# Kernel tuning notes

Hardware: AMD Instinct MI355X
Metric: run time of the kernel (lower is better)

Reference implementation:

```python
import jax, jax.numpy as jnp
import numpy as np

T = 8192
F = 128   # feature_size
H = 2048  # hidden_size
PRED_LEN = 12  # pred_length (fc_out head exists in module but is unused in forward)


def setup_inputs() -> dict:
    key = jax.random.key(0)
    ks = jax.random.split(key, 10)
    s_ih = 1.0 / np.sqrt(H)
    inp = {
        "x": jax.random.normal(ks[0], (T, F), dtype=jnp.float32),
        # PyTorch nn.LSTM params, gate order [i, f, g, o]
        "W_ih": jax.random.uniform(ks[1], (4 * H, F), jnp.float32, -s_ih, s_ih),
        "W_hh": jax.random.uniform(ks[2], (4 * H, H), jnp.float32, -s_ih, s_ih),
        "b_ih": jax.random.uniform(ks[3], (4 * H,), jnp.float32, -s_ih, s_ih),
        "b_hh": jax.random.uniform(ks[4], (4 * H,), jnp.float32, -s_ih, s_ih),
        # self.linear: Linear(H, H)
        "W_lin": jax.random.uniform(ks[5], (H, H), jnp.float32, -s_ih, s_ih),
        "b_lin": jax.random.uniform(ks[6], (H,), jnp.float32, -s_ih, s_ih),
        # self.one_out: Linear(H, 2)
        "W_out": jax.random.uniform(ks[7], (2, H), jnp.float32, -s_ih, s_ih),
        "b_out": jax.random.uniform(ks[8], (2,), jnp.float32, -s_ih, s_ih),
    }
    return inp


def _lstm_last_h(x, W_ih, W_hh, b_ih, b_hh):
    # x: [T, F]; returns final hidden state h: [H]
    # Precompute input projections for all timesteps: [T, 4H]
    x_proj = x @ W_ih.T + (b_ih + b_hh)

    def step(carry, xp):
        h, c = carry
        gates = xp + h @ W_hh.T  # [4H]
        i = jax.nn.sigmoid(gates[0 * H:1 * H])
        f = jax.nn.sigmoid(gates[1 * H:2 * H])
        g = jnp.tanh(gates[2 * H:3 * H])
        o = jax.nn.sigmoid(gates[3 * H:4 * H])
        c = f * c + i * g
        h = o * jnp.tanh(c)
        return (h, c), None

    h0 = jnp.zeros((H,), x.dtype)
    c0 = jnp.zeros((H,), x.dtype)
    (h, _), _ = jax.lax.scan(step, (h0, c0), x_proj)
    return h


def reference(x, W_ih, W_hh, b_ih, b_hh, W_lin, b_lin, W_out, b_out):
    h = _lstm_last_h(x, W_ih, W_hh, b_ih, b_hh)        # [H]
    y = h @ W_lin.T + b_lin                            # [H]
    y = y @ W_out.T + b_out                            # [2]
    return y.reshape(1, 1, 2)                          # matches torch (1,1,2)
```

## Files before the change

kernel.cpp:

```cpp
#include <hip/hip_runtime.h>


#define H      2048
#define TSTEPS 8192
#define FEAT   128
#define NBLK   256
#define NTHR   512

typedef float vf4 __attribute__((ext_vector_type(4)));
typedef float vf2 __attribute__((ext_vector_type(2)));
typedef unsigned long long u64;
typedef unsigned int u32;

__device__ __forceinline__ float sigm(float xv) {
  return __builtin_amdgcn_rcpf(1.0f + __expf(-xv));
}
__device__ __forceinline__ float tanh_(float xv) {
  return 1.0f - 2.0f * __builtin_amdgcn_rcpf(__expf(2.0f * xv) + 1.0f);
}

__device__ __forceinline__ u64 aload64(const u64* p) {
  return __hip_atomic_load(p, __ATOMIC_RELAXED, __HIP_MEMORY_SCOPE_AGENT);
}
__device__ __forceinline__ u32 aload32(const u32* p) {
  return __hip_atomic_load(p, __ATOMIC_RELAXED, __HIP_MEMORY_SCOPE_AGENT);
}
__device__ __forceinline__ void astoref(float* p, float v) {
  __hip_atomic_store(p, v, __ATOMIC_RELAXED, __HIP_MEMORY_SCOPE_AGENT);
}
__device__ __forceinline__ void astoreu(u32* p, u32 v) {
  __hip_atomic_store(p, v, __ATOMIC_RELAXED, __HIP_MEMORY_SCOPE_AGENT);
}

#define DECLG(g) vf4 w##g##_0, w##g##_1, w##g##_2, w##g##_3, \
                     w##g##_4, w##g##_5, w##g##_6, w##g##_7; \
                 vf2 wih##g; float bias##g; float acc##g;

#define LOADG(g) { \
  const int row_ = (g) * H + j; \
  const float* wr_ = W_hh + (long)row_ * H; \
  w##g##_0 = *(const vf4*)(wr_ + 4*(ln      )); \
  w##g##_1 = *(const vf4*)(wr_ + 4*(ln +  64)); \
  w##g##_2 = *(const vf4*)(wr_ + 4*(ln + 128)); \
  w##g##_3 = *(const vf4*)(wr_ + 4*(ln + 192)); \
  w##g##_4 = *(const vf4*)(wr_ + 4*(ln + 256)); \
  w##g##_5 = *(const vf4*)(wr_ + 4*(ln + 320)); \
  w##g##_6 = *(const vf4*)(wr_ + 4*(ln + 384)); \
  w##g##_7 = *(const vf4*)(wr_ + 4*(ln + 448)); \
  wih##g  = *(const vf2*)(W_ih + (long)row_ * FEAT + 2*ln); \
  bias##g = b_ih[row_] + b_hh[row_]; }

#define PIN(g) asm volatile("" : \
  "+v"(w##g##_0), "+v"(w##g##_1), "+v"(w##g##_2), "+v"(w##g##_3), \
  "+v"(w##g##_4), "+v"(w##g##_5), "+v"(w##g##_6), "+v"(w##g##_7), \
  "+v"(wih##g), "+v"(bias##g));

#define LDSREAD(k, ldsrow) \
  const vf4 hv##k = *(const vf4*)&(ldsrow)[4*(ln + 64*(k))];

#define FMA_G(g, c) \
  acc##g = __builtin_fmaf(w##g##_##c.x, h4_.x, acc##g); \
  acc##g = __builtin_fmaf(w##g##_##c.y, h4_.y, acc##g); \
  acc##g = __builtin_fmaf(w##g##_##c.z, h4_.z, acc##g); \
  acc##g = __builtin_fmaf(w##g##_##c.w, h4_.w, acc##g);

#define FMA_C(c) { const vf4 h4_ = hv##c; \
  FMA_G(0, c) FMA_G(1, c) FMA_G(2, c) FMA_G(3, c) }

#define REDUCE(g) { float a_ = acc##g; \
  a_ += __shfl_xor(a_, 1);  a_ += __shfl_xor(a_, 2);  a_ += __shfl_xor(a_, 4); \
  a_ += __shfl_xor(a_, 8);  a_ += __shfl_xor(a_, 16); a_ += __shfl_xor(a_, 32); \
  acc##g = a_ + bias##g; }

__device__ __forceinline__ void poll_and_stage(const u32* __restrict__ slots,
                                               const float* __restrict__ hsrc,
                                               int tgt,
                                               float* __restrict__ ldsrow,
                                               int wv, int ln) {
  const u32* sp = slots + wv * 32 + (ln & 31);
  int v = (int)aload32(sp);
  while (!__all((ln < 32) ? (v >= tgt) : 1)) {
    __builtin_amdgcn_s_sleep(1);
    if ((ln < 32) && (v < tgt)) v = (int)aload32(sp);
  }
  const int base = wv * 256 + 4 * ln;
  const u64* hp = (const u64*)(hsrc + base);
  const u64 d0 = aload64(hp);
  const u64 d1 = aload64(hp + 1);
  vf4 hv;
  hv.x = __uint_as_float((u32)d0);
  hv.y = __uint_as_float((u32)(d0 >> 32));
  hv.z = __uint_as_float((u32)d1);
  hv.w = __uint_as_float((u32)(d1 >> 32));
  *(vf4*)&ldsrow[base] = hv;
}

__global__ __launch_bounds__(NTHR, 2)
void lstm_persist(const float* __restrict__ x,
                  const float* __restrict__ W_ih,
                  const float* __restrict__ W_hh,
                  const float* __restrict__ b_ih,
                  const float* __restrict__ b_hh,
                  const float* __restrict__ W_lin,
                  const float* __restrict__ b_lin,
                  const float* __restrict__ W_out,
                  const float* __restrict__ b_out,
                  float* __restrict__ out,
                  float* __restrict__ ws)
{
  const int tid = threadIdx.x;
  const int b   = blockIdx.x;
  const int wv  = tid >> 6;
  const int ln  = tid & 63;

  float* hbuf0 = ws;
  float* hbuf1 = ws + H;
  u32*   slots = (u32*)(ws + 2 * H);

  __shared__ __align__(16) float h_lds[2][H];

  *(vf4*)&h_lds[0][4 * tid] = (vf4)(0.0f);

  const int j = b * 8 + wv;
  DECLG(0) DECLG(1) DECLG(2) DECLG(3)
  LOADG(0) LOADG(1) LOADG(2) LOADG(3)
  PIN(0) PIN(1) PIN(2) PIN(3)

  __syncthreads();

  float cst = 0.0f;

  #pragma unroll 1
  for (int t = 0; t < TSTEPS; ++t) {
    const vf2 xr = *(const vf2*)(x + (long)t * FEAT + 2 * ln);
    float* ldsrow = h_lds[t & 1];

    if (t > 0)
      poll_and_stage(slots, (t & 1) ? hbuf1 : hbuf0, t, ldsrow, wv, ln);
    __syncthreads();

    LDSREAD(0, ldsrow) LDSREAD(1, ldsrow) LDSREAD(2, ldsrow) LDSREAD(3, ldsrow)
    LDSREAD(4, ldsrow) LDSREAD(5, ldsrow) LDSREAD(6, ldsrow) LDSREAD(7, ldsrow)

    acc0 = wih0.x * xr.x + wih0.y * xr.y;
    acc1 = wih1.x * xr.x + wih1.y * xr.y;
    acc2 = wih2.x * xr.x + wih2.y * xr.y;
    acc3 = wih3.x * xr.x + wih3.y * xr.y;

    FMA_C(0) FMA_C(1) FMA_C(2) FMA_C(3)
    FMA_C(4) FMA_C(5) FMA_C(6) FMA_C(7)

    REDUCE(0) REDUCE(1) REDUCE(2) REDUCE(3)

    const float iv = sigm(acc0);
    const float fv = sigm(acc1);
    const float gv = tanh_(acc2);
    const float ov = sigm(acc3);
    cst = fv * cst + iv * gv;
    const float hval = ov * tanh_(cst);

    if (ln == 0)
      astoref((((t + 1) & 1) ? hbuf1 : hbuf0) + j, hval);

    __syncthreads();
    if (tid == 0)
      astoreu(slots + b, (u32)(t + 1));
  }

  {
    float* ldsrow = h_lds[0];
    poll_and_stage(slots, hbuf0, TSTEPS, ldsrow, wv, ln);
    __syncthreads();

    float a0 = 0.0f;
    const float* wl = W_lin + (long)j * H;
    #pragma unroll
    for (int k = 0; k < 8; ++k) {
      const vf4 h4 = *(const vf4*)&ldsrow[4 * (ln + 64 * k)];
      const vf4 u  = *(const vf4*)(wl + 4 * (ln + 64 * k));
      a0 += u.x * h4.x + u.y * h4.y + u.z * h4.z + u.w * h4.w;
    }
    a0 += __shfl_xor(a0, 1);  a0 += __shfl_xor(a0, 2);  a0 += __shfl_xor(a0, 4);
    a0 += __shfl_xor(a0, 8);  a0 += __shfl_xor(a0, 16); a0 += __shfl_xor(a0, 32);

    if (ln == 0)
      astoref(hbuf1 + j, a0 + b_lin[j]);
    __syncthreads();
    if (tid == 0)
      astoreu(slots + b, (u32)(TSTEPS + 1));
  }

  if (b == 0 && wv == 0) {
    const u32* sp = slots + 4 * ln;
    int v0 = (int)aload32(sp + 0), v1 = (int)aload32(sp + 1);
    int v2 = (int)aload32(sp + 2), v3 = (int)aload32(sp + 3);
    const int tgt = TSTEPS + 1;
    while (!__all((v0 >= tgt) & (v1 >= tgt) & (v2 >= tgt) & (v3 >= tgt))) {
      __builtin_amdgcn_s_sleep(1);
      if (v0 < tgt) v0 = (int)aload32(sp + 0);
      if (v1 < tgt) v1 = (int)aload32(sp + 1);
      if (v2 < tgt) v2 = (int)aload32(sp + 2);
      if (v3 < tgt) v3 = (int)aload32(sp + 3);
    }
    float p0 = 0.0f, p1 = 0.0f;
    #pragma unroll
    for (int k = 0; k < 16; ++k) {
      const u64 d  = aload64((const u64*)hbuf1 + ln + 64 * k);
      const int c  = 2 * (ln + 64 * k);
      const float ylo = __uint_as_float((u32)d);
      const float yhi = __uint_as_float((u32)(d >> 32));
      p0 = __builtin_fmaf(W_out[c],         ylo, p0);
      p0 = __builtin_fmaf(W_out[c + 1],     yhi, p0);
      p1 = __builtin_fmaf(W_out[H + c],     ylo, p1);
      p1 = __builtin_fmaf(W_out[H + c + 1], yhi, p1);
    }
    p0 += __shfl_xor(p0, 1);  p0 += __shfl_xor(p0, 2);  p0 += __shfl_xor(p0, 4);
    p0 += __shfl_xor(p0, 8);  p0 += __shfl_xor(p0, 16); p0 += __shfl_xor(p0, 32);
    p1 += __shfl_xor(p1, 1);  p1 += __shfl_xor(p1, 2);  p1 += __shfl_xor(p1, 4);
    p1 += __shfl_xor(p1, 8);  p1 += __shfl_xor(p1, 16); p1 += __shfl_xor(p1, 32);
    if (ln == 0) {
      out[0] = p0 + b_out[0];
      out[1] = p1 + b_out[1];
    }
  }
}

extern "C" void kernel_launch(void* const* d_in, const int* in_sizes, int n_in,
                              void* d_out, int out_size, void* d_ws, size_t ws_size,
                              hipStream_t stream) {
  const float* x     = (const float*)d_in[0];
  const float* W_ih  = (const float*)d_in[1];
  const float* W_hh  = (const float*)d_in[2];
  const float* b_ih  = (const float*)d_in[3];
  const float* b_hh  = (const float*)d_in[4];
  const float* W_lin = (const float*)d_in[5];
  const float* b_lin = (const float*)d_in[6];
  const float* W_out = (const float*)d_in[7];
  const float* b_out = (const float*)d_in[8];

  lstm_persist<<<dim3(NBLK), dim3(NTHR), 0, stream>>>(
      x, W_ih, W_hh, b_ih, b_hh, W_lin, b_lin, W_out, b_out,
      (float*)d_out, (float*)d_ws);
}
```

Baseline: 34.44 ms.

## Replace per-block flags with step-tagged 64-bit hidden-state entries

Each hidden value is now written together with its timestep tag as one 64-bit atomic store. Consumers poll the tagged data directly instead of first polling per-block flags and then reading the data. This drops the per-step block barrier and the separate flag store, cutting one dependent global round trip from the critical path of every recurrent step. In exchange, each wave's polling now reads 4 u64 per lane instead of one u32, which raises spin traffic to L2, and the workspace footprint doubles.

Result: slower. 48.50 ms (+40.8%).

```diff
diff --git a/kernel.cpp b/kernel.cpp
--- a/kernel.cpp
+++ b/kernel.cpp
@@ -22,14 +22,13 @@
 __device__ __forceinline__ u64 aload64(const u64* p) {
   return __hip_atomic_load(p, __ATOMIC_RELAXED, __HIP_MEMORY_SCOPE_AGENT);
 }
-__device__ __forceinline__ u32 aload32(const u32* p) {
-  return __hip_atomic_load(p, __ATOMIC_RELAXED, __HIP_MEMORY_SCOPE_AGENT);
-}
-__device__ __forceinline__ void astoref(float* p, float v) {
+__device__ __forceinline__ void astore64(u64* p, u64 v) {
   __hip_atomic_store(p, v, __ATOMIC_RELAXED, __HIP_MEMORY_SCOPE_AGENT);
 }
-__device__ __forceinline__ void astoreu(u32* p, u32 v) {
-  __hip_atomic_store(p, v, __ATOMIC_RELAXED, __HIP_MEMORY_SCOPE_AGENT);
+__device__ __forceinline__ int  tag_of(u64 d) { return (int)(u32)(d >> 32); }
+__device__ __forceinline__ float val_of(u64 d) { return __uint_as_float((u32)d); }
+__device__ __forceinline__ u64  pack(int tag, float v) {
+  return ((u64)(u32)tag << 32) | (u64)__float_as_uint(v);
 }
 
 #define DECLG(g) vf4 w##g##_0, w##g##_1, w##g##_2, w##g##_3, \
@@ -72,27 +71,29 @@
   a_ += __shfl_xor(a_, 8);  a_ += __shfl_xor(a_, 16); a_ += __shfl_xor(a_, 32); \
   acc##g = a_ + bias##g; }
 
-__device__ __forceinline__ void poll_and_stage(const u32* __restrict__ slots,
-                                               const float* __restrict__ hsrc,
-                                               int tgt,
-                                               float* __restrict__ ldsrow,
-                                               int wv, int ln) {
-  const u32* sp = slots + wv * 32 + (ln & 31);
-  int v = (int)aload32(sp);
-  while (!__all((ln < 32) ? (v >= tgt) : 1)) {
+__device__ __forceinline__ void poll_stage(const u64* __restrict__ pq,
+                                           int tgt,
+                                           float* __restrict__ ldsrow,
+                                           int wv, int ln) {
+  const u64* hp = pq + wv * 256 + 4 * ln;
+  u64 d0 = aload64(hp + 0);
+  u64 d1 = aload64(hp + 1);
+  u64 d2 = aload64(hp + 2);
+  u64 d3 = aload64(hp + 3);
+  while (!__all((tag_of(d0) >= tgt) & (tag_of(d1) >= tgt) &
+                (tag_of(d2) >= tgt) & (tag_of(d3) >= tgt))) {
     __builtin_amdgcn_s_sleep(1);
-    if ((ln < 32) && (v < tgt)) v = (int)aload32(sp);
-  }
-  const int base = wv * 256 + 4 * ln;
-  const u64* hp = (const u64*)(hsrc + base);
-  const u64 d0 = aload64(hp);
-  const u64 d1 = aload64(hp + 1);
+    if (tag_of(d0) < tgt) d0 = aload64(hp + 0);
+    if (tag_of(d1) < tgt) d1 = aload64(hp + 1);
+    if (tag_of(d2) < tgt) d2 = aload64(hp + 2);
+    if (tag_of(d3) < tgt) d3 = aload64(hp + 3);
+  }
   vf4 hv;
-  hv.x = __uint_as_float((u32)d0);
-  hv.y = __uint_as_float((u32)(d0 >> 32));
-  hv.z = __uint_as_float((u32)d1);
-  hv.w = __uint_as_float((u32)(d1 >> 32));
-  *(vf4*)&ldsrow[base] = hv;
+  hv.x = val_of(d0);
+  hv.y = val_of(d1);
+  hv.z = val_of(d2);
+  hv.w = val_of(d3);
+  *(vf4*)&ldsrow[wv * 256 + 4 * ln] = hv;
 }
 
 __global__ __launch_bounds__(NTHR, 2)
@@ -113,9 +114,7 @@
   const int wv  = tid >> 6;
   const int ln  = tid & 63;
 
-  float* hbuf0 = ws;
-  float* hbuf1 = ws + H;
-  u32*   slots = (u32*)(ws + 2 * H);
+  u64* hq = (u64*)ws;
 
   __shared__ __align__(16) float h_lds[2][H];
 
@@ -136,7 +135,7 @@
     float* ldsrow = h_lds[t & 1];
 
     if (t > 0)
-      poll_and_stage(slots, (t & 1) ? hbuf1 : hbuf0, t, ldsrow, wv, ln);
+      poll_stage(hq + (t & 1) * H, t, ldsrow, wv, ln);
     __syncthreads();
 
     LDSREAD(0, ldsrow) LDSREAD(1, ldsrow) LDSREAD(2, ldsrow) LDSREAD(3, ldsrow)
@@ -160,16 +159,12 @@
     const float hval = ov * tanh_(cst);
 
     if (ln == 0)
-      astoref((((t + 1) & 1) ? hbuf1 : hbuf0) + j, hval);
-
-    __syncthreads();
-    if (tid == 0)
-      astoreu(slots + b, (u32)(t + 1));
+      astore64(hq + ((t + 1) & 1) * H + j, pack(t + 1, hval));
   }
 
   {
     float* ldsrow = h_lds[0];
-    poll_and_stage(slots, hbuf0, TSTEPS, ldsrow, wv, ln);
+    poll_stage(hq, TSTEPS, ldsrow, wv, ln);
     __syncthreads();
 
     float a0 = 0.0f;
@@ -184,35 +179,39 @@
     a0 += __shfl_xor(a0, 8);  a0 += __shfl_xor(a0, 16); a0 += __shfl_xor(a0, 32);
 
     if (ln == 0)
-      astoref(hbuf1 + j, a0 + b_lin[j]);
-    __syncthreads();
-    if (tid == 0)
-      astoreu(slots + b, (u32)(TSTEPS + 1));
+      astore64(hq + H + j, pack(TSTEPS + 1, a0 + b_lin[j]));
   }
 
   if (b == 0 && wv == 0) {
-    const u32* sp = slots + 4 * ln;
-    int v0 = (int)aload32(sp + 0), v1 = (int)aload32(sp + 1);
-    int v2 = (int)aload32(sp + 2), v3 = (int)aload32(sp + 3);
+    const u64* yq = hq + H;
     const int tgt = TSTEPS + 1;
-    while (!__all((v0 >= tgt) & (v1 >= tgt) & (v2 >= tgt) & (v3 >= tgt))) {
-      __builtin_amdgcn_s_sleep(1);
-      if (v0 < tgt) v0 = (int)aload32(sp + 0);
-      if (v1 < tgt) v1 = (int)aload32(sp + 1);
-      if (v2 < tgt) v2 = (int)aload32(sp + 2);
-      if (v3 < tgt) v3 = (int)aload32(sp + 3);
-    }
     float p0 = 0.0f, p1 = 0.0f;
-    #pragma unroll
-    for (int k = 0; k < 16; ++k) {
-      const u64 d  = aload64((const u64*)hbuf1 + ln + 64 * k);
-      const int c  = 2 * (ln + 64 * k);
-      const float ylo = __uint_as_float((u32)d);
-      const float yhi = __uint_as_float((u32)(d >> 32));
-      p0 = __builtin_fmaf(W_out[c],         ylo, p0);
-      p0 = __builtin_fmaf(W_out[c + 1],     yhi, p0);
-      p1 = __builtin_fmaf(W_out[H + c],     ylo, p1);
-      p1 = __builtin_fmaf(W_out[H + c + 1], yhi, p1);
+    #pragma unroll 1
+    for (int kb = 0; kb < 8; ++kb) {
+      const u64* q = yq + kb * 256 + 4 * ln;
+      u64 e0 = aload64(q + 0);
+      u64 e1 = aload64(q + 1);
+      u64 e2 = aload64(q + 2);
+      u64 e3 = aload64(q + 3);
+      while (!__all((tag_of(e0) >= tgt) & (tag_of(e1) >= tgt) &
+                    (tag_of(e2) >= tgt) & (tag_of(e3) >= tgt))) {
+        __builtin_amdgcn_s_sleep(1);
+        if (tag_of(e0) < tgt) e0 = aload64(q + 0);
+        if (tag_of(e1) < tgt) e1 = aload64(q + 1);
+        if (tag_of(e2) < tgt) e2 = aload64(q + 2);
+        if (tag_of(e3) < tgt) e3 = aload64(q + 3);
+      }
+      const int c = kb * 256 + 4 * ln;
+      const float y0 = val_of(e0), y1 = val_of(e1);
+      const float y2 = val_of(e2), y3 = val_of(e3);
+      p0 = __builtin_fmaf(W_out[c + 0],     y0, p0);
+      p0 = __builtin_fmaf(W_out[c + 1],     y1, p0);
+      p0 = __builtin_fmaf(W_out[c + 2],     y2, p0);
+      p0 = __builtin_fmaf(W_out[c + 3],     y3, p0);
+      p1 = __builtin_fmaf(W_out[H + c + 0], y0, p1);
+      p1 = __builtin_fmaf(W_out[H + c + 1], y1, p1);
+      p1 = __builtin_fmaf(W_out[H + c + 2], y2, p1);
+      p1 = __builtin_fmaf(W_out[H + c + 3], y3, p1);
     }
     p0 += __shfl_xor(p0, 1);  p0 += __shfl_xor(p0, 2);  p0 += __shfl_xor(p0, 4);
     p0 += __shfl_xor(p0, 8);  p0 += __shfl_xor(p0, 16); p0 += __shfl_xor(p0, 32);
```

## Replace end-of-step barrier with LDS atomic counter and busy-burn polling

Applied to the files above, without the earlier changes.

Drops the per-step __syncthreads before publishing the block's step flag. Each wave now waits for its own h store (vmcnt(0)) and increments a shared LDS counter, and the last of the 8 waves publishes the flag. The s_sleep in the polling loops is replaced with a chain of dependent FMAs, which is meant to keep polling latency short and the clock up. In exchange it adds LDS atomics, spends ALU power while spinning, and publishing the flag after only a wait on the wave's own store relies on memory-ordering assumptions that could be fragile.

Measured after the change: 50.41 ms. +46.4%, slower.

```diff
diff --git a/kernel.cpp b/kernel.cpp
--- a/kernel.cpp
+++ b/kernel.cpp
@@ -31,6 +31,11 @@
 __device__ __forceinline__ void astoreu(u32* p, u32 v) {
   __hip_atomic_store(p, v, __ATOMIC_RELAXED, __HIP_MEMORY_SCOPE_AGENT);
 }
+
+#define BURN(z) { \
+  _Pragma("unroll") \
+  for (int u_ = 0; u_ < 48; ++u_) (z) = __builtin_fmaf((z), 1.0000001f, 1e-30f); \
+  asm volatile("" : "+v"(z)); }
 
 #define DECLG(g) vf4 w##g##_0, w##g##_1, w##g##_2, w##g##_3, \
                      w##g##_4, w##g##_5, w##g##_6, w##g##_7; \
@@ -76,13 +81,17 @@
                                                const float* __restrict__ hsrc,
                                                int tgt,
                                                float* __restrict__ ldsrow,
-                                               int wv, int ln) {
+                                               int wv, int ln, float* zz) {
   const u32* sp = slots + wv * 32 + (ln & 31);
-  int v = (int)aload32(sp);
-  while (!__all((ln < 32) ? (v >= tgt) : 1)) {
-    __builtin_amdgcn_s_sleep(1);
-    if ((ln < 32) && (v < tgt)) v = (int)aload32(sp);
-  }
+  int v = (ln < 32) ? (int)aload32(sp) : 0x7fffffff;
+  float z = *zz;
+  while (!__all(v >= tgt)) {
+    int nv = v;
+    if ((ln < 32) && (v < tgt)) nv = (int)aload32(sp);
+    BURN(z)
+    v = nv;
+  }
+  *zz = z;
   const int base = wv * 256 + 4 * ln;
   const u64* hp = (const u64*)(hsrc + base);
   const u64 d0 = aload64(hp);
@@ -118,8 +127,10 @@
   u32*   slots = (u32*)(ws + 2 * H);
 
   __shared__ __align__(16) float h_lds[2][H];
+  __shared__ int pub_cnt;
 
   *(vf4*)&h_lds[0][4 * tid] = (vf4)(0.0f);
+  if (tid == 0) pub_cnt = 0;
 
   const int j = b * 8 + wv;
   DECLG(0) DECLG(1) DECLG(2) DECLG(3)
@@ -129,6 +140,7 @@
   __syncthreads();
 
   float cst = 0.0f;
+  float zburn = 1.0f;
 
   #pragma unroll 1
   for (int t = 0; t < TSTEPS; ++t) {
@@ -136,7 +148,7 @@
     float* ldsrow = h_lds[t & 1];
 
     if (t > 0)
-      poll_and_stage(slots, (t & 1) ? hbuf1 : hbuf0, t, ldsrow, wv, ln);
+      poll_and_stage(slots, (t & 1) ? hbuf1 : hbuf0, t, ldsrow, wv, ln, &zburn);
     __syncthreads();
 
     LDSREAD(0, ldsrow) LDSREAD(1, ldsrow) LDSREAD(2, ldsrow) LDSREAD(3, ldsrow)
@@ -161,15 +173,17 @@
 
     if (ln == 0)
       astoref((((t + 1) & 1) ? hbuf1 : hbuf0) + j, hval);
-
-    __syncthreads();
-    if (tid == 0)
-      astoreu(slots + b, (u32)(t + 1));
+    asm volatile("s_waitcnt vmcnt(0)" ::: "memory");
+    if (ln == 0) {
+      const int old = atomicAdd(&pub_cnt, 1);
+      if (old == 8 * t + 7)
+        astoreu(slots + b, (u32)(t + 1));
+    }
   }
 
   {
     float* ldsrow = h_lds[0];
-    poll_and_stage(slots, hbuf0, TSTEPS, ldsrow, wv, ln);
+    poll_and_stage(slots, hbuf0, TSTEPS, ldsrow, wv, ln, &zburn);
     __syncthreads();
 
     float a0 = 0.0f;
@@ -195,12 +209,15 @@
     int v0 = (int)aload32(sp + 0), v1 = (int)aload32(sp + 1);
     int v2 = (int)aload32(sp + 2), v3 = (int)aload32(sp + 3);
     const int tgt = TSTEPS + 1;
+    float z = zburn;
     while (!__all((v0 >= tgt) & (v1 >= tgt) & (v2 >= tgt) & (v3 >= tgt))) {
-      __builtin_amdgcn_s_sleep(1);
-      if (v0 < tgt) v0 = (int)aload32(sp + 0);
-      if (v1 < tgt) v1 = (int)aload32(sp + 1);
-      if (v2 < tgt) v2 = (int)aload32(sp + 2);
-      if (v3 < tgt) v3 = (int)aload32(sp + 3);
+      int n0 = v0, n1 = v1, n2 = v2, n3 = v3;
+      if (v0 < tgt) n0 = (int)aload32(sp + 0);
+      if (v1 < tgt) n1 = (int)aload32(sp + 1);
+      if (v2 < tgt) n2 = (int)aload32(sp + 2);
+      if (v3 < tgt) n3 = (int)aload32(sp + 3);
+      BURN(z)
+      v0 = n0; v1 = n1; v2 = n2; v3 = n3;
     }
     float p0 = 0.0f, p1 = 0.0f;
     #pragma unroll
```

## Halve block count and let one wave poll global flags per block

Applied to the files above, without the earlier changes.

Moves the persistent LSTM kernel from 256 blocks of 512 threads to 128 blocks of 1024 threads, so each block owns 16 hidden units and the grid barrier involves half as many participants. Global polling of step counters now runs in wave 0 only, which then sets a workgroup-scoped LDS flag that the other waves spin on before each stages its slice of h. The aim is to cut cross-block barrier latency and global polling traffic on each of the 8192 serial steps. The cost is an extra intra-block handoff and busy-spinning waves, and the 1024-thread blocks with launch bounds of 4 put more pressure on register allocation for the pinned weight registers.

New measurement: 56.99 ms. 1.65x slower.

```diff
diff --git a/kernel.cpp b/kernel.cpp
--- a/kernel.cpp
+++ b/kernel.cpp
@@ -4,8 +4,9 @@
 #define H      2048
 #define TSTEPS 8192
 #define FEAT   128
-#define NBLK   256
-#define NTHR   512
+#define NBLK   128
+#define NTHR   1024
+#define UPB    16
 
 typedef float vf4 __attribute__((ext_vector_type(4)));
 typedef float vf2 __attribute__((ext_vector_type(2)));
@@ -30,6 +31,12 @@
 }
 __device__ __forceinline__ void astoreu(u32* p, u32 v) {
   __hip_atomic_store(p, v, __ATOMIC_RELAXED, __HIP_MEMORY_SCOPE_AGENT);
+}
+__device__ __forceinline__ void flag_store(int* f, int v) {
+  __hip_atomic_store(f, v, __ATOMIC_RELAXED, __HIP_MEMORY_SCOPE_WORKGROUP);
+}
+__device__ __forceinline__ int flag_load(const int* f) {
+  return __hip_atomic_load(f, __ATOMIC_RELAXED, __HIP_MEMORY_SCOPE_WORKGROUP);
 }
 
 #define DECLG(g) vf4 w##g##_0, w##g##_1, w##g##_2, w##g##_3, \
@@ -72,30 +79,35 @@
   a_ += __shfl_xor(a_, 8);  a_ += __shfl_xor(a_, 16); a_ += __shfl_xor(a_, 32); \
   acc##g = a_ + bias##g; }
 
-__device__ __forceinline__ void poll_and_stage(const u32* __restrict__ slots,
-                                               const float* __restrict__ hsrc,
-                                               int tgt,
-                                               float* __restrict__ ldsrow,
-                                               int wv, int ln) {
-  const u32* sp = slots + wv * 32 + (ln & 31);
-  int v = (int)aload32(sp);
-  while (!__all((ln < 32) ? (v >= tgt) : 1)) {
-    __builtin_amdgcn_s_sleep(1);
-    if ((ln < 32) && (v < tgt)) v = (int)aload32(sp);
-  }
-  const int base = wv * 256 + 4 * ln;
-  const u64* hp = (const u64*)(hsrc + base);
-  const u64 d0 = aload64(hp);
-  const u64 d1 = aload64(hp + 1);
-  vf4 hv;
-  hv.x = __uint_as_float((u32)d0);
-  hv.y = __uint_as_float((u32)(d0 >> 32));
-  hv.z = __uint_as_float((u32)d1);
-  hv.w = __uint_as_float((u32)(d1 >> 32));
-  *(vf4*)&ldsrow[base] = hv;
-}
-
-__global__ __launch_bounds__(NTHR, 2)
+__device__ __forceinline__ void gate_wait(const u32* __restrict__ slots,
+                                          int tgt, int wv, int ln, int* flag) {
+  if (wv == 0) {
+    const u32* sp = slots + ln;
+    int v0 = (int)aload32(sp);
+    int v1 = (int)aload32(sp + 64);
+    while (!__all((v0 >= tgt) & (v1 >= tgt))) {
+      __builtin_amdgcn_s_sleep(1);
+      if (v0 < tgt) v0 = (int)aload32(sp);
+      if (v1 < tgt) v1 = (int)aload32(sp + 64);
+    }
+    if (ln == 0) flag_store(flag, tgt);
+  } else {
+    while (flag_load(flag) < tgt) { }
+  }
+}
+
+__device__ __forceinline__ void stage_slice(const float* __restrict__ hsrc,
+                                            float* __restrict__ ldsrow,
+                                            int wv, int ln) {
+  const int base = wv * 128 + 2 * ln;
+  const u64 d = aload64((const u64*)(hsrc + base));
+  vf2 hv;
+  hv.x = __uint_as_float((u32)d);
+  hv.y = __uint_as_float((u32)(d >> 32));
+  *(vf2*)&ldsrow[base] = hv;
+}
+
+__global__ __launch_bounds__(NTHR, 4)
 void lstm_persist(const float* __restrict__ x,
                   const float* __restrict__ W_ih,
                   const float* __restrict__ W_hh,
@@ -118,10 +130,12 @@
   u32*   slots = (u32*)(ws + 2 * H);
 
   __shared__ __align__(16) float h_lds[2][H];
-
-  *(vf4*)&h_lds[0][4 * tid] = (vf4)(0.0f);
-
-  const int j = b * 8 + wv;
+  __shared__ int flag;
+
+  *(vf2*)&h_lds[0][2 * tid] = (vf2)(0.0f);
+  if (tid == 0) flag = 0;
+
+  const int j = b * UPB + wv;
   DECLG(0) DECLG(1) DECLG(2) DECLG(3)
   LOADG(0) LOADG(1) LOADG(2) LOADG(3)
   PIN(0) PIN(1) PIN(2) PIN(3)
@@ -135,8 +149,10 @@
     const vf2 xr = *(const vf2*)(x + (long)t * FEAT + 2 * ln);
     float* ldsrow = h_lds[t & 1];
 
-    if (t > 0)
-      poll_and_stage(slots, (t & 1) ? hbuf1 : hbuf0, t, ldsrow, wv, ln);
+    if (t > 0) {
+      gate_wait(slots, t, wv, ln, &flag);
+      stage_slice((t & 1) ? hbuf1 : hbuf0, ldsrow, wv, ln);
+    }
     __syncthreads();
 
     LDSREAD(0, ldsrow) LDSREAD(1, ldsrow) LDSREAD(2, ldsrow) LDSREAD(3, ldsrow)
@@ -161,7 +177,6 @@
 
     if (ln == 0)
       astoref((((t + 1) & 1) ? hbuf1 : hbuf0) + j, hval);
-
     __syncthreads();
     if (tid == 0)
       astoreu(slots + b, (u32)(t + 1));
@@ -169,7 +184,8 @@
 
   {
     float* ldsrow = h_lds[0];
-    poll_and_stage(slots, hbuf0, TSTEPS, ldsrow, wv, ln);
+    gate_wait(slots, TSTEPS, wv, ln, &flag);
+    stage_slice(hbuf0, ldsrow, wv, ln);
     __syncthreads();
 
     float a0 = 0.0f;
@@ -191,16 +207,14 @@
   }
 
   if (b == 0 && wv == 0) {
-    const u32* sp = slots + 4 * ln;
-    int v0 = (int)aload32(sp + 0), v1 = (int)aload32(sp + 1);
-    int v2 = (int)aload32(sp + 2), v3 = (int)aload32(sp + 3);
+    const u32* sp = slots + ln;
+    int v0 = (int)aload32(sp);
+    int v1 = (int)aload32(sp + 64);
     const int tgt = TSTEPS + 1;
-    while (!__all((v0 >= tgt) & (v1 >= tgt) & (v2 >= tgt) & (v3 >= tgt))) {
+    while (!__all((v0 >= tgt) & (v1 >= tgt))) {
       __builtin_amdgcn_s_sleep(1);
-      if (v0 < tgt) v0 = (int)aload32(sp + 0);
-      if (v1 < tgt) v1 = (int)aload32(sp + 1);
-      if (v2 < tgt) v2 = (int)aload32(sp + 2);
-      if (v3 < tgt) v3 = (int)aload32(sp + 3);
+      if (v0 < tgt) v0 = (int)aload32(sp);
+      if (v1 < tgt) v1 = (int)aload32(sp + 64);
     }
     float p0 = 0.0f, p1 = 0.0f;
     #pragma unroll
```
